# Kernel optimization log

Measured on AMD Instinct MI355X. Metric: run time of the kernel, lower is better.

Reference implementation:

```python
import jax, jax.numpy as jnp
import numpy as np

N_NODES = 50000
N_EDGES = 600000
N_GRAPHS = 512
HID = 128
LAT = 64
L = 4
BN_EPS = 1e-5


def _gelu(x):
    return jax.nn.gelu(x, approximate=False)


def _bn(x, g, b):
    m = jnp.mean(x, axis=0)
    v = jnp.var(x, axis=0)
    return (x - m) * jax.lax.rsqrt(v + BN_EPS) * g + b


def setup_inputs() -> dict:
    key = jax.random.key(0)
    ks = jax.random.split(key, 8)
    x = jax.random.normal(ks[0], (N_NODES, HID), dtype=jnp.float32)
    edge_index = jax.random.randint(ks[1], (2, N_EDGES), 0, N_NODES, dtype=jnp.int64 if jax.config.jax_enable_x64 else jnp.int32)
    batch = jnp.sort(jax.random.randint(ks[2], (N_NODES,), 0, N_GRAPHS))
    scale = 1.0 / np.sqrt(HID)
    return {
        "x": x,
        "edge_index": edge_index,
        "batch": batch,
        "input_bn_g": jnp.ones((HID,), jnp.float32),
        "input_bn_b": jnp.zeros((HID,), jnp.float32),
        "eps": jnp.zeros((L,), jnp.float32),
        "fc1_w": jax.random.normal(ks[3], (L, HID, HID), jnp.float32) * scale,
        "fc1_b": jnp.zeros((L, HID), jnp.float32),
        "bn1_g": jnp.ones((L, HID), jnp.float32),
        "bn1_b": jnp.zeros((L, HID), jnp.float32),
        "fc2_w": jax.random.normal(ks[4], (L, HID, HID), jnp.float32) * scale,
        "fc2_b": jnp.zeros((L, HID), jnp.float32),
        "bn_g": jnp.ones((L, HID), jnp.float32),
        "bn_b": jnp.zeros((L, HID), jnp.float32),
        "att_weight": jax.random.normal(ks[5], (L, HID), jnp.float32),
        "pool_weight": jnp.ones((3,), jnp.float32),
        "fcA_w": jax.random.normal(ks[6], (HID, HID), jnp.float32) * scale,
        "fcA_b": jnp.zeros((HID,), jnp.float32),
        "ln_g": jnp.ones((HID,), jnp.float32),
        "ln_b": jnp.zeros((HID,), jnp.float32),
        "fcB_w": jax.random.normal(ks[7], (HID, LAT), jnp.float32) * scale,
        "fcB_b": jnp.zeros((LAT,), jnp.float32),
    }


def reference(x, edge_index, batch, input_bn_g, input_bn_b, eps, fc1_w, fc1_b,
              bn1_g, bn1_b, fc2_w, fc2_b, bn_g, bn_b, att_weight, pool_weight,
              fcA_w, fcA_b, ln_g, ln_b, fcB_w, fcB_b):
    src, dst = edge_index[0], edge_index[1]
    x = _bn(x, input_bn_g, input_bn_b)  # input BatchNorm (batch stats)
    hidden_states = []
    for l in range(L):
        # GINConv: (1+eps)*x_i + sum_{j->i} x_j, then GatedResidualMLP
        agg = jax.ops.segment_sum(x[src], dst, num_segments=N_NODES)
        h = (1.0 + eps[l]) * x + agg
        h = _gelu(_bn(h @ fc1_w[l] + fc1_b[l], bn1_g[l], bn1_b[l]))
        h = h @ fc2_w[l] + fc2_b[l]
        h = _gelu(_bn(h, bn_g[l], bn_b[l]))
        hidden_states.append(h)
        x = h
    # JumpingKnowledge attention over layers
    x_all = jnp.stack(hidden_states, axis=0)               # [L, N, H]
    scores = jnp.mean(x_all * att_weight[:, None, :], -1)  # [L, N]
    alpha = jax.nn.softmax(scores, axis=0)
    x = jnp.sum(x_all * alpha[..., None], axis=0)          # [N, H]
    # fused add/mean/max pooling by graph id
    pw = jax.nn.softmax(pool_weight)
    sums = jax.ops.segment_sum(x, batch, num_segments=N_GRAPHS)
    cnt = jax.ops.segment_sum(jnp.ones((N_NODES, 1), x.dtype), batch, num_segments=N_GRAPHS)
    mean = sums / jnp.maximum(cnt, 1.0)
    mx = jax.ops.segment_max(x, batch, num_segments=N_GRAPHS)
    mx = jnp.where(cnt > 0, mx, 0.0)
    pooled = sums * pw[0] + mean * pw[1] + mx * pw[2]      # [G, H]
    out = pooled @ fcA_w + fcA_b
    mu = jnp.mean(out, -1, keepdims=True)
    var = jnp.var(out, -1, keepdims=True)
    out = (out - mu) * jax.lax.rsqrt(var + 1e-5) * ln_g + ln_b
    out = _gelu(out) + pooled
    return out @ fcB_w + fcB_b                              # [G, latent]
```

## Files before the change

### kernel.cpp

```cpp
#include <hip/hip_runtime.h>
#include <math.h>

#define N_NODES 50000
#define N_EDGES 600000
#define N_GRAPHS 512
#define HID 128
#define LAT 64
#define NL 4
#define SSTR 16
#define SSET 4096
#define N_TILES 3125
#define TLD 72

typedef __attribute__((ext_vector_type(8))) __bf16 bf16x8;
typedef __attribute__((ext_vector_type(4))) float f32x4;

union Chunk {
    bf16x8 v;
    uint4 u4;
    ushort us[8];
};

__device__ __forceinline__ float gelu_exact(float x) {
    return 0.5f * x * (1.0f + erff(x * 0.70710678118654752f));
}
__device__ __forceinline__ float gelu_fast(float x) {
    float ax = fabsf(x) * 0.70710678118654752f;
    float t = __builtin_amdgcn_rcpf(fmaf(0.3275911f, ax, 1.0f));
    float p = t * (0.254829592f +
              t * (-0.284496736f +
              t * (1.421413741f +
              t * (-1.453152027f + t * 1.061405429f))));
    float e = __expf(-ax * ax);
    float erfv = 1.0f - p * e;
    float erfs = copysignf(erfv, x);
    return 0.5f * x * (1.0f + erfs);
}
__device__ __forceinline__ float bf2f(ushort h) {
    return __uint_as_float(((unsigned int)h) << 16);
}
__device__ __forceinline__ ushort f2bf(float f) {
    unsigned int u = __float_as_uint(f);
    unsigned int r = (u + 0x7FFFu + ((u >> 16) & 1u)) >> 16;
    return (ushort)r;
}

__device__ __forceinline__ void part_range(int p, int& r0, int& r1) {
    r0 = (p * N_NODES) >> 8;
    r1 = ((p + 1) * N_NODES) >> 8;
}
__device__ __forceinline__ void sub_range(int p, int j, int& s0, int& s1) {
    int r0, r1;
    part_range(p, r0, r1);
    int len = r1 - r0;
    s0 = r0 + ((len * j) >> 3);
    s1 = r0 + ((len * (j + 1)) >> 3);
}

__global__ __launch_bounds__(256) void wt_build(const float* __restrict__ fc1w,
                                                const float* __restrict__ fc2w,
                                                ushort* __restrict__ Wt) {
    int i = blockIdx.x * 256 + threadIdx.x;
    if (i >= 8 * HID * HID) return;
    int g = i >> 14;
    int rem = i & 16383;
    int n = rem >> 7, k = rem & 127;
    const float* W = (g < 4) ? (fc1w + (long)g * HID * HID) : (fc2w + (long)(g - 4) * HID * HID);
    Wt[i] = f2bf(W[k * HID + n]);
}

__global__ __launch_bounds__(256) void col_stats(const float* __restrict__ X,
                                                 float* __restrict__ stats) {
    __shared__ float sh[2048];
    int t = threadIdx.x;
    int tx = t & 31, ty = t >> 5;
    float s[4] = {0, 0, 0, 0}, q[4] = {0, 0, 0, 0};
    const int nTiles = (N_NODES + 63) / 64;
    for (int tile = blockIdx.x; tile < nTiles; tile += gridDim.x) {
        int r0 = tile * 64;
#pragma unroll
        for (int i = 0; i < 8; ++i) {
            int r = r0 + ty + 8 * i;
            int rc = min(r, N_NODES - 1);
            float4 v = *(const float4*)(X + (long)rc * HID + 4 * tx);
            float w = (r < N_NODES) ? 1.f : 0.f;
            float x0 = v.x * w, x1 = v.y * w, x2 = v.z * w, x3 = v.w * w;
// ... 26 lines not shown
                                                    ushort* __restrict__ Y,
                                                    const float* __restrict__ stats,
                                                    const float* __restrict__ g,
                                                    const float* __restrict__ b) {
    __shared__ float scL[HID], sfL[HID];
    int t = threadIdx.x;
    if (t < HID) {
        const float invN = 1.0f / (float)N_NODES;
        float mean = stats[t * SSTR] * invN;
        float var = stats[(HID + t) * SSTR] * invN - mean * mean;
        float s = g[t] * rsqrtf(var + 1e-5f);
        scL[t] = s;
        sfL[t] = b[t] - mean * s;
    }
    __syncthreads();
    int c4 = (t & 31) * 4;
    float sc[4], sf[4];
#pragma unroll
    for (int j = 0; j < 4; ++j) { sc[j] = scL[c4 + j]; sf[j] = sfL[c4 + j]; }
    int s0, s1;
    sub_range(blockIdx.x & 255, blockIdx.x >> 8, s0, s1);
    int c0 = s0 * 32, c1 = s1 * 32;
    for (int i = c0 + t; i < c1; i += 256) {
        float4 v = ((const float4*)X)[i];
        ushort4 w;
        w.x = f2bf(v.x * sc[0] + sf[0]);
        w.y = f2bf(v.y * sc[1] + sf[1]);
        w.z = f2bf(v.z * sc[2] + sf[2]);
        w.w = f2bf(v.w * sc[3] + sf[3]);
        ((ushort4*)Y)[i] = w;
    }
}

__global__ __launch_bounds__(256) void bn_apply_bf(const ushort* __restrict__ X,
                                                   ushort* __restrict__ Y,
                                                   const float* __restrict__ stats,
                                                   const float* __restrict__ g,
                                                   const float* __restrict__ b) {
    __shared__ float scL[HID], sfL[HID];
    int t = threadIdx.x;
    if (t < HID) {
        const float invN = 1.0f / (float)N_NODES;
        float mean = stats[t * SSTR] * invN;
        float var = stats[(HID + t) * SSTR] * invN - mean * mean;
        float s = g[t] * rsqrtf(var + 1e-5f);
        scL[t] = s;
        sfL[t] = b[t] - mean * s;
    }
    __syncthreads();
    int c8 = (t & 15) * 8;
    float sc[8], sf[8];
#pragma unroll
    for (int j = 0; j < 8; ++j) { sc[j] = scL[c8 + j]; sf[j] = sfL[c8 + j]; }
    int s0, s1;
    sub_range(blockIdx.x & 255, blockIdx.x >> 8, s0, s1);
    int c0 = s0 * 16, c1 = s1 * 16;
    for (int i = c0 + t; i < c1; i += 256) {
        Chunk ch;
        ch.u4 = ((const uint4*)X)[i];
#pragma unroll
        for (int j = 0; j < 8; ++j) {
            float f = bf2f(ch.us[j]) * sc[j] + sf[j];
            ch.us[j] = f2bf(gelu_fast(f));
        }
        ((uint4*)Y)[i] = ch.u4;
    }
}

__global__ __launch_bounds__(256) void csr_count(const int* __restrict__ dst,
                                                 int* __restrict__ counts) {
    int e = blockIdx.x * blockDim.x + threadIdx.x;
    if (e >= N_EDGES) return;
    atomicAdd(counts + dst[e], 1);
}

__global__ __launch_bounds__(256) void scan_pass1(const int* __restrict__ counts,
                                                  int* __restrict__ offs,
                                                  int* __restrict__ bsum) {
    __shared__ int sh[256];
    int t = threadIdx.x;
    int i = blockIdx.x * 256 + t;
    int v = (i < N_NODES) ? counts[i] : 0;
    sh[t] = v;
    __syncthreads();
    for (int off = 1; off < 256; off <<= 1) {
        int a = (t >= off) ? sh[t - off] : 0;
        __syncthreads();
        sh[t] += a;
        __syncthreads();
    }
    if (i < N_NODES) offs[i] = sh[t] - v;
    if (t == 255) bsum[blockIdx.x] = sh[255];
}

__global__ __launch_bounds__(256) void scan_pass2(int* __restrict__ bsum, int nblk) {
    __shared__ int sh[256];
    int t = threadIdx.x;
    int v = (t < nblk) ? bsum[t] : 0;
    sh[t] = v;
    __syncthreads();
    for (int off = 1; off < 256; off <<= 1) {
        int a = (t >= off) ? sh[t - off] : 0;
        __syncthreads();
        sh[t] += a;
        __syncthreads();
    }
    if (t < nblk) bsum[t] = sh[t] - v;
}

__global__ __launch_bounds__(256) void scan_pass3(int* __restrict__ offs,
                                                  const int* __restrict__ bsum,
                                                  int* __restrict__ cursor) {
    int i = blockIdx.x * 256 + threadIdx.x;
    if (i >= N_NODES) return;
    int o = offs[i] + bsum[blockIdx.x];
    offs[i] = o;
    cursor[i] = o;
}

__global__ __launch_bounds__(256) void csr_fill(const int* __restrict__ src,
                                                const int* __restrict__ dst,
                                                int* __restrict__ cursor,
                                                int* __restrict__ csr) {
    int e = blockIdx.x * blockDim.x + threadIdx.x;
    if (e >= N_EDGES) return;
    int pos = atomicAdd(cursor + dst[e], 1);
    csr[pos] = src[e];
}

__global__ __launch_bounds__(256) void gin_gather_bf(const ushort* __restrict__ Xbf,
                                                     ushort* __restrict__ Hp,
                                                     const int* __restrict__ offs,
                                                     const int* __restrict__ counts,
                                                     const int* __restrict__ csr,
                                                     const float* __restrict__ eps, int l) {
    int t = threadIdx.x;
    int tx = t & 31;
    int g = t >> 5;
    int s0, s1;
    sub_range(blockIdx.x & 255, blockIdx.x >> 8, s0, s1);
    float ev = 1.0f + eps[l];
    for (int node = s0 + g; node < s1; node += 8) {
        ushort4 sv = *(const ushort4*)(Xbf + (long)node * HID + 4 * tx);
        float a0 = bf2f(sv.x) * ev, a1 = bf2f(sv.y) * ev;
        float a2 = bf2f(sv.z) * ev, a3 = bf2f(sv.w) * ev;
        int o = offs[node];
        int d = counts[node];
        int k = 0;
        for (; k + 8 <= d; k += 8) {
            int si[8];
#pragma unroll
            for (int j = 0; j < 8; ++j) si[j] = csr[o + k + j];
            ushort4 v[8];
#pragma unroll
            for (int j = 0; j < 8; ++j)
                v[j] = *(const ushort4*)(Xbf + (long)si[j] * HID + 4 * tx);
#pragma unroll
            for (int j = 0; j < 8; ++j) {
                a0 += bf2f(v[j].x); a1 += bf2f(v[j].y);
                a2 += bf2f(v[j].z); a3 += bf2f(v[j].w);
            }
        }
        for (; k + 4 <= d; k += 4) {
            int si[4];
#pragma unroll
            for (int j = 0; j < 4; ++j) si[j] = csr[o + k + j];
#pragma unroll
            for (int j = 0; j < 4; ++j) {
                ushort4 v = *(const ushort4*)(Xbf + (long)si[j] * HID + 4 * tx);
                a0 += bf2f(v.x); a1 += bf2f(v.y); a2 += bf2f(v.z); a3 += bf2f(v.w);
            }
        }
        for (; k < d; ++k) {
            int s = csr[o + k];
            ushort4 v = *(const ushort4*)(Xbf + (long)s * HID + 4 * tx);
            a0 += bf2f(v.x); a1 += bf2f(v.y); a2 += bf2f(v.z); a3 += bf2f(v.w);
        }
        ushort4 w;
        w.x = f2bf(a0); w.y = f2bf(a1); w.z = f2bf(a2); w.w = f2bf(a3);
        *(ushort4*)(Hp + (long)node * HID + 4 * tx) = w;
    }
}

__global__ __launch_bounds__(256, 1) void gemm_persist(
    const ushort* __restrict__ Abf, const ushort* __restrict__ Wt,
    const float* __restrict__ bias, ushort* __restrict__ Cbf,
    const float* __restrict__ statsIn, const float* __restrict__ gIn,
    const float* __restrict__ bIn, int applyIn, float* __restrict__ statsOut) {
    __shared__ float scL[HID], sfL[HID];
    __shared__ __align__(16) ushort T[4][16 * TLD];
    __shared__ float shs[8 * 64];
    int t = threadIdx.x;
    if (applyIn && t < HID) {
        const float invN = 1.0f / (float)N_NODES;
        float mean = statsIn[t * SSTR] * invN;
        float var = statsIn[(HID + t) * SSTR] * invN - mean * mean;
        float s = gIn[t] * rsqrtf(var + 1e-5f);
        scL[t] = s;
        sfL[t] = bIn[t] - mean * s;
    }
    __syncthreads();

    int w = t >> 6, lane = t & 63;
    int m = lane & 15, q = lane >> 4;
    int c2 = w & 1, r2 = w >> 1;
    ushort* Tw = T[w];

    const ushort* Wh = Wt + (long)(c2 * 64) * HID;
    bf16x8 Bfrag[4][4];
#pragma unroll
    for (int nt = 0; nt < 4; ++nt)
#pragma unroll
        for (int kc = 0; kc < 4; ++kc)
            Bfrag[nt][kc] = *(const bf16x8*)(Wh + (nt * 16 + m) * HID + kc * 32 + q * 8);

    float bias4[4];
#pragma unroll
    for (int nt = 0; nt < 4; ++nt) bias4[nt] = bias[c2 * 64 + nt * 16 + m];

    float s_col[4], q_col[4];
#pragma unroll
    for (int nt = 0; nt < 4; ++nt) { s_col[nt] = 0.f; q_col[nt] = 0.f; }

    int t0 = (blockIdx.x * N_TILES) >> 8;
    int t1 = ((blockIdx.x + 1) * N_TILES) >> 8;

    int tile = t0 + r2;
    Chunk Ac[4];
    if (tile < t1) {
        const ushort* arow = Abf + (long)(tile * 16 + m) * HID + q * 8;
#pragma unroll
        for (int kc = 0; kc < 4; ++kc) Ac[kc].u4 = *(const uint4*)(arow + kc * 32);
    }
    while (tile < t1) {
        int nxt = tile + 2;
        Chunk An[4];
        if (nxt < t1) {
            const ushort* arow = Abf + (long)(nxt * 16 + m) * HID + q * 8;
#pragma unroll
            for (int kc = 0; kc < 4; ++kc) An[kc].u4 = *(const uint4*)(arow + kc * 32);
        }
        if (applyIn) {
#pragma unroll
            for (int kc = 0; kc < 4; ++kc)
#pragma unroll
                for (int j = 0; j < 8; ++j) {
                    int k = kc * 32 + q * 8 + j;
                    float f = bf2f(Ac[kc].us[j]) * scL[k] + sfL[k];
                    Ac[kc].us[j] = f2bf(gelu_fast(f));
                }
        }
        f32x4 acc[4];
#pragma unroll
        for (int nt = 0; nt < 4; ++nt) acc[nt] = (f32x4){0.f, 0.f, 0.f, 0.f};
#pragma unroll
        for (int kc = 0; kc < 4; ++kc)
#pragma unroll
            for (int nt = 0; nt < 4; ++nt)
// ... 17 lines not shown
            int row = slot >> 3, off = slot & 7;
            uint4 vv = *(const uint4*)(Tw + row * TLD + off * 8);
            *(uint4*)(Cbf + cbase + (long)row * HID + off * 8) = vv;
        }
        tile = nxt;
#pragma unroll
        for (int kc = 0; kc < 4; ++kc) Ac[kc] = An[kc];
    }

#pragma unroll
    for (int nt = 0; nt < 4; ++nt) {
        s_col[nt] += __shfl_xor(s_col[nt], 16);
        s_col[nt] += __shfl_xor(s_col[nt], 32);
        q_col[nt] += __shfl_xor(q_col[nt], 16);
        q_col[nt] += __shfl_xor(q_col[nt], 32);
    }
    if (q == 0) {
#pragma unroll
        for (int nt = 0; nt < 4; ++nt) {
            shs[w * 64 + nt * 16 + m] = s_col[nt];
            shs[256 + w * 64 + nt * 16 + m] = q_col[nt];
        }
    }
    __syncthreads();
    if (t < HID) {
        int half = t >> 6, lc = t & 63;
        float a = shs[half * 64 + lc] + shs[(2 + half) * 64 + lc];
        float b = shs[256 + half * 64 + lc] + shs[256 + (2 + half) * 64 + lc];
        atomicAdd(statsOut + t * SSTR, a);
        atomicAdd(statsOut + (HID + t) * SSTR, b);
    }
}

__global__ __launch_bounds__(256) void jk_attn_bf(const ushort* __restrict__ H0,
                                                  const ushort* __restrict__ H1,
                                                  const ushort* __restrict__ H2,
                                                  const ushort* __restrict__ H3,
                                                  const float* __restrict__ att,
                                                  float* __restrict__ Y) {
    int t = threadIdx.x;
    int lane = t & 63, w = t >> 6;
    int s0, s1;
    sub_range(blockIdx.x & 255, blockIdx.x >> 8, s0, s1);
    const ushort* Hs[4] = {H0, H1, H2, H3};
    float2 av[4];
#pragma unroll
    for (int l = 0; l < 4; ++l) av[l] = *(const float2*)(att + l * HID + 2 * lane);
    for (int node = s0 + w; node < s1; node += 4) {
        float hx[4], hy[4], sc[4];
#pragma unroll
        for (int l = 0; l < 4; ++l) {
            unsigned int u = *(const unsigned int*)(Hs[l] + (long)node * HID + 2 * lane);
            float vx = bf2f((ushort)(u & 0xFFFF));
            float vy = bf2f((ushort)(u >> 16));
            hx[l] = vx; hy[l] = vy;
            float p = vx * av[l].x + vy * av[l].y;
#pragma unroll
            for (int off = 32; off > 0; off >>= 1) p += __shfl_xor(p, off);
            sc[l] = p * (1.0f / HID);
        }
        float mm = fmaxf(fmaxf(sc[0], sc[1]), fmaxf(sc[2], sc[3]));
        float e[4], se = 0.f;
#pragma unroll
        for (int l = 0; l < 4; ++l) { e[l] = expf(sc[l] - mm); se += e[l]; }
        float inv = 1.0f / se;
        float ox = 0.f, oy = 0.f;
#pragma unroll
        for (int l = 0; l < 4; ++l) {
            float a = e[l] * inv;
            ox += a * hx[l];
            oy += a * hy[l];
        }
        *(float2*)(Y + (long)node * HID + 2 * lane) = make_float2(ox, oy);
    }
}

__global__ void graph_ranges(const int* __restrict__ batch, int* __restrict__ gstart,
                             int* __restrict__ gend) {
    int n = blockIdx.x * blockDim.x + threadIdx.x;
    if (n >= N_NODES) return;
    int b = batch[n];
    if (n == 0 || batch[n - 1] != b) gstart[b] = n;
    if (n == N_NODES - 1 || batch[n + 1] != b) gend[b] = n + 1;
}

__global__ __launch_bounds__(128) void pool_kernel(const float* __restrict__ X,
                                                   const int* __restrict__ gstart,
                                                   const int* __restrict__ gend,
                                                   const float* __restrict__ pw,
                                                   float* __restrict__ pooled) {
    int g = blockIdx.x;
    int f = threadIdx.x;
    float w0 = pw[0], w1 = pw[1], w2 = pw[2];
    float m = fmaxf(w0, fmaxf(w1, w2));
    float e0 = expf(w0 - m), e1 = expf(w1 - m), e2 = expf(w2 - m);
    float inv = 1.0f / (e0 + e1 + e2);
    e0 *= inv; e1 *= inv; e2 *= inv;
    int s = gstart[g], e = gend[g];
    float sum = 0.f, mx = -INFINITY;
    for (int n = s; n < e; ++n) {
        float v = X[(long)n * HID + f];
        sum += v;
        mx = fmaxf(mx, v);
    }
    int cnt = e - s;
    float mean = cnt > 0 ? sum / (float)cnt : 0.f;
    float mxv = cnt > 0 ? mx : 0.f;
    pooled[g * HID + f] = sum * e0 + mean * e1 + mxv * e2;
}

__global__ __launch_bounds__(128) void head_kernel(const float* __restrict__ pooled,
                                                   const float* __restrict__ fcAw,
                                                   const float* __restrict__ fcAb,
                                                   const float* __restrict__ lng,
                                                   const float* __restrict__ lnb,
                                                   const float* __restrict__ fcBw,
                                                   const float* __restrict__ fcBb,
                                                   float* __restrict__ out) {
    __shared__ float p[HID], q[HID], red[HID];
    int g = blockIdx.x, j = threadIdx.x;
    p[j] = pooled[g * HID + j];
    __syncthreads();
    float acc = fcAb[j];
    for (int k = 0; k < HID; ++k) acc += p[k] * fcAw[k * HID + j];
    red[j] = acc;
    __syncthreads();
    for (int off = 64; off > 0; off >>= 1) {
        if (j < off) red[j] += red[j + off];
        __syncthreads();
    }
    float mean = red[0] * (1.0f / HID);
    __syncthreads();
    float d = acc - mean;
    red[j] = d * d;
    __syncthreads();
    for (int off = 64; off > 0; off >>= 1) {
        if (j < off) red[j] += red[j + off];
        __syncthreads();
    }
    float var = red[0] * (1.0f / HID);
    float y = d * rsqrtf(var + 1e-5f) * lng[j] + lnb[j];
// ... 8 lines not shown

extern "C" void kernel_launch(void* const* d_in, const int* in_sizes, int n_in,
                              void* d_out, int out_size, void* d_ws, size_t ws_size,
                              hipStream_t stream) {
    const float* x = (const float*)d_in[0];
    const int* ei = (const int*)d_in[1];
    const int* src = ei;
    const int* dst = ei + N_EDGES;
    const int* batch = (const int*)d_in[2];
    const float* ibn_g = (const float*)d_in[3];
    const float* ibn_b = (const float*)d_in[4];
    const float* eps = (const float*)d_in[5];
    const float* fc1w = (const float*)d_in[6];
    const float* fc1b = (const float*)d_in[7];
    const float* bn1g = (const float*)d_in[8];
    const float* bn1b = (const float*)d_in[9];
    const float* fc2w = (const float*)d_in[10];
    const float* fc2b = (const float*)d_in[11];
    const float* bng = (const float*)d_in[12];
    const float* bnb = (const float*)d_in[13];
    const float* att = (const float*)d_in[14];
    const float* pw = (const float*)d_in[15];
    const float* fcAw = (const float*)d_in[16];
    const float* fcAb = (const float*)d_in[17];
    const float* lng = (const float*)d_in[18];
    const float* lnb = (const float*)d_in[19];
    const float* fcBw = (const float*)d_in[20];
    const float* fcBb = (const float*)d_in[21];
    float* out = (float*)d_out;

    const size_t NH = (size_t)N_NODES * HID;
    char* w8 = (char*)d_ws;
    ushort* x0bf = (ushort*)w8;     w8 += NH * 2;
    ushort* hprebf = (ushort*)w8;   w8 += NH * 2;
    ushort* z1bf = (ushort*)w8;     w8 += NH * 2;
    ushort* Hlbf[NL];
    for (int l = 0; l < NL; ++l) { Hlbf[l] = (ushort*)w8; w8 += NH * 2; }
    float* ztmp = (float*)w8;       w8 += NH * 4;
    float* statsAll = (float*)w8;   w8 += (size_t)9 * SSET * 4;
    float* pooled = (float*)w8;     w8 += (size_t)N_GRAPHS * HID * 4;
    int* gstart = (int*)w8;         w8 += N_GRAPHS * 4;
    int* gend = (int*)w8;           w8 += N_GRAPHS * 4;
    int* counts = (int*)w8;         w8 += N_NODES * 4;
    int* offs = (int*)w8;           w8 += N_NODES * 4;
    int* cursor = (int*)w8;         w8 += N_NODES * 4;
    int* bsum = (int*)w8;           w8 += 256 * 4;
    int* csr = (int*)w8;            w8 += (size_t)N_EDGES * 4;
    ushort* WtBf = (ushort*)w8;     w8 += (size_t)8 * HID * HID * 2;

    const int nodeBlocks = (N_NODES + 255) / 256;
    const int edgeBlocks = (N_EDGES + 255) / 256;

    wt_build<<<512, 256, 0, stream>>>(fc1w, fc2w, WtBf);

    hipMemsetAsync(counts, 0, N_NODES * sizeof(int), stream);
    csr_count<<<edgeBlocks, 256, 0, stream>>>(dst, counts);
    scan_pass1<<<nodeBlocks, 256, 0, stream>>>(counts, offs, bsum);
    scan_pass2<<<1, 256, 0, stream>>>(bsum, nodeBlocks);
    scan_pass3<<<nodeBlocks, 256, 0, stream>>>(offs, bsum, cursor);
    csr_fill<<<edgeBlocks, 256, 0, stream>>>(src, dst, cursor, csr);

    hipMemsetAsync(statsAll, 0, (size_t)9 * SSET * sizeof(float), stream);

    col_stats<<<256, 256, 0, stream>>>(x, statsAll);
    bn_apply_f32<<<2048, 256, 0, stream>>>(x, x0bf, statsAll, ibn_g, ibn_b);

    const ushort* xin = x0bf;
    for (int l = 0; l < NL; ++l) {
        float* st1 = statsAll + (size_t)(1 + 2 * l) * SSET;
        float* st2 = statsAll + (size_t)(2 + 2 * l) * SSET;
        gin_gather_bf<<<2048, 256, 0, stream>>>(xin, hprebf, offs, counts, csr, eps, l);
        gemm_persist<<<256, 256, 0, stream>>>(hprebf, WtBf + (size_t)l * HID * HID,
                                              fc1b + l * HID, z1bf,
                                              nullptr, nullptr, nullptr, 0, st1);
        gemm_persist<<<256, 256, 0, stream>>>(z1bf, WtBf + (size_t)(4 + l) * HID * HID,
                                              fc2b + l * HID, hprebf,
                                              st1, bn1g + l * HID, bn1b + l * HID, 1, st2);
        bn_apply_bf<<<2048, 256, 0, stream>>>(hprebf, Hlbf[l], st2, bng + l * HID,
                                              bnb + l * HID);
        xin = Hlbf[l];
    }

    jk_attn_bf<<<2048, 256, 0, stream>>>(Hlbf[0], Hlbf[1], Hlbf[2], Hlbf[3], att, ztmp);

    hipMemsetAsync(gstart, 0, 2 * N_GRAPHS * sizeof(int), stream);
    graph_ranges<<<nodeBlocks, 256, 0, stream>>>(batch, gstart, gend);
    pool_kernel<<<N_GRAPHS, 128, 0, stream>>>(ztmp, gstart, gend, pw, pooled);

    head_kernel<<<N_GRAPHS, 128, 0, stream>>>(pooled, fcAw, fcAb, lng, lnb, fcBw, fcBb, out);
}
```

Before: 557.8 us.

## Fuse GIN neighbor gather into first per-layer GEMM with MFMA

Replaces the separate gather kernel plus first persistent GEMM with one kernel in which each thread aggregates a full node row (its own features scaled by 1+eps, plus its neighbors) straight into MFMA A-fragments, then multiplies by register-resident weight fragments and accumulates BN statistics. This removes the write and re-read of the aggregated hidden buffer and one launch per layer. In exchange, each block redoes its weight-fragment loads, uses launch_bounds(256,1), and gathers with one thread per row at 16-byte width, which may hide latency worse than the old warp-per-node gather and is hit by degree imbalance within a wave.

```diff
diff --git a/kernel.cpp b/kernel.cpp
--- a/kernel.cpp
+++ b/kernel.cpp
@@ -10,6 +10,7 @@
 #define SSTR 16
 #define SSET 4096
 #define N_TILES 3125
+#define N_GG 1563
 #define TLD 72
 
 typedef __attribute__((ext_vector_type(8))) __bf16 bf16x8;
@@ -45,13 +46,9 @@
     return (ushort)r;
 }
 
-__device__ __forceinline__ void part_range(int p, int& r0, int& r1) {
-    r0 = (p * N_NODES) >> 8;
-    r1 = ((p + 1) * N_NODES) >> 8;
-}
 __device__ __forceinline__ void sub_range(int p, int j, int& s0, int& s1) {
-    int r0, r1;
-    part_range(p, r0, r1);
+    int r0 = (p * N_NODES) >> 8;
+    int r1 = ((p + 1) * N_NODES) >> 8;
     int len = r1 - r0;
     s0 = r0 + ((len * j) >> 3);
     s1 = r0 + ((len * (j + 1)) >> 3);
@@ -240,57 +237,141 @@
     csr[pos] = src[e];
 }
 
-__global__ __launch_bounds__(256) void gin_gather_bf(const ushort* __restrict__ Xbf,
-                                                     ushort* __restrict__ Hp,
-                                                     const int* __restrict__ offs,
-                                                     const int* __restrict__ counts,
-                                                     const int* __restrict__ csr,
-                                                     const float* __restrict__ eps, int l) {
+__global__ __launch_bounds__(256, 1) void gather_gemm(
+    const ushort* __restrict__ Xbf, const int* __restrict__ offs,
+    const int* __restrict__ counts, const int* __restrict__ csr,
+    const float* __restrict__ eps, int l,
+    const ushort* __restrict__ Wt, const float* __restrict__ bias,
+    ushort* __restrict__ Cbf, float* __restrict__ statsOut) {
+    __shared__ __align__(16) ushort T[4][16 * TLD];
+    __shared__ float shs[8 * 64];
     int t = threadIdx.x;
-    int tx = t & 31;
-    int g = t >> 5;
-    int s0, s1;
-    sub_range(blockIdx.x & 255, blockIdx.x >> 8, s0, s1);
+    int w = t >> 6, lane = t & 63;
+    int m = lane & 15, q = lane >> 4;
+    int c2 = w & 1, r2 = w >> 1;
+    ushort* Tw = T[w];
+
+    const ushort* Wh = Wt + (long)(c2 * 64) * HID;
+    bf16x8 Bfrag[4][4];
+#pragma unroll
+    for (int nt = 0; nt < 4; ++nt)
+#pragma unroll
+        for (int kc = 0; kc < 4; ++kc)
+            Bfrag[nt][kc] = *(const bf16x8*)(Wh + (nt * 16 + m) * HID + kc * 32 + q * 8);
+
+    float bias4[4];
+#pragma unroll
+    for (int nt = 0; nt < 4; ++nt) bias4[nt] = bias[c2 * 64 + nt * 16 + m];
+
     float ev = 1.0f + eps[l];
-    for (int node = s0 + g; node < s1; node += 8) {
-        ushort4 sv = *(const ushort4*)(Xbf + (long)node * HID + 4 * tx);
-        float a0 = bf2f(sv.x) * ev, a1 = bf2f(sv.y) * ev;
-        float a2 = bf2f(sv.z) * ev, a3 = bf2f(sv.w) * ev;
-        int o = offs[node];
-        int d = counts[node];
-        int k = 0;
-        for (; k + 8 <= d; k += 8) {
-            int si[8];
-#pragma unroll
-            for (int j = 0; j < 8; ++j) si[j] = csr[o + k + j];
-            ushort4 v[8];
+    int rbase = blockIdx.x * 32 + r2 * 16;
+    int row = rbase + m;
+    int valid = row < N_NODES;
+    int rowc = valid ? row : N_NODES - 1;
+
+    float accf[4][8];
+    {
+        const ushort* xr = Xbf + (long)rowc * HID + q * 8;
+        Chunk ch[4];
+#pragma unroll
+        for (int kc = 0; kc < 4; ++kc) ch[kc].u4 = *(const uint4*)(xr + kc * 32);
+#pragma unroll
+        for (int kc = 0; kc < 4; ++kc)
+#pragma unroll
+            for (int j = 0; j < 8; ++j) accf[kc][j] = bf2f(ch[kc].us[j]) * ev;
+    }
+    int d = valid ? counts[row] : 0;
+    int o = valid ? offs[row] : 0;
+    int k = 0;
+    for (; k + 2 <= d; k += 2) {
+        int s0 = csr[o + k], s1 = csr[o + k + 1];
+        const ushort* p0 = Xbf + (long)s0 * HID + q * 8;
+        const ushort* p1 = Xbf + (long)s1 * HID + q * 8;
+        Chunk a0[4], a1[4];
+#pragma unroll
+        for (int kc = 0; kc < 4; ++kc) {
+            a0[kc].u4 = *(const uint4*)(p0 + kc * 32);
+            a1[kc].u4 = *(const uint4*)(p1 + kc * 32);
+        }
+#pragma unroll
+        for (int kc = 0; kc < 4; ++kc)
 #pragma unroll
             for (int j = 0; j < 8; ++j)
-                v[j] = *(const ushort4*)(Xbf + (long)si[j] * HID + 4 * tx);
-#pragma unroll
-            for (int j = 0; j < 8; ++j) {
-                a0 += bf2f(v[j].x); a1 += bf2f(v[j].y);
-                a2 += bf2f(v[j].z); a3 += bf2f(v[j].w);
+                accf[kc][j] += bf2f(a0[kc].us[j]) + bf2f(a1[kc].us[j]);
+    }
+    if (k < d) {
+        int s0 = csr[o + k];
+        const ushort* p0 = Xbf + (long)s0 * HID + q * 8;
+        Chunk a0[4];
+#pragma unroll
+        for (int kc = 0; kc < 4; ++kc) a0[kc].u4 = *(const uint4*)(p0 + kc * 32);
+#pragma unroll
+        for (int kc = 0; kc < 4; ++kc)
+#pragma unroll
+            for (int j = 0; j < 8; ++j) accf[kc][j] += bf2f(a0[kc].us[j]);
+    }
+
+    Chunk Af[4];
+#pragma unroll
+    for (int kc = 0; kc < 4; ++kc)
+#pragma unroll
+        for (int j = 0; j < 8; ++j) Af[kc].us[j] = f2bf(accf[kc][j]);
+
+    f32x4 acc[4];
+#pragma unroll
+    for (int nt = 0; nt < 4; ++nt) acc[nt] = (f32x4){0.f, 0.f, 0.f, 0.f};
+#pragma unroll
+    for (int kc = 0; kc < 4; ++kc)
+#pragma unroll
+        for (int nt = 0; nt < 4; ++nt)
+            acc[nt] = __builtin_amdgcn_mfma_f32_16x16x32_bf16(Af[kc].v, Bfrag[nt][kc],
+                                                              acc[nt], 0, 0, 0);
+
+    float s_col[4] = {0, 0, 0, 0}, q_col[4] = {0, 0, 0, 0};
+#pragma unroll
+    for (int nt = 0; nt < 4; ++nt) {
+        int col = nt * 16 + m;
+#pragma unroll
+        for (int r = 0; r < 4; ++r) {
+            float z = acc[nt][r] + bias4[nt];
+            Tw[(q * 4 + r) * TLD + col] = f2bf(z);
+            if (rbase + q * 4 + r < N_NODES) {
+                s_col[nt] += z;
+                q_col[nt] += z * z;
             }
         }
-        for (; k + 4 <= d; k += 4) {
-            int si[4];
-#pragma unroll
-            for (int j = 0; j < 4; ++j) si[j] = csr[o + k + j];
-#pragma unroll
-            for (int j = 0; j < 4; ++j) {
-                ushort4 v = *(const ushort4*)(Xbf + (long)si[j] * HID + 4 * tx);
-                a0 += bf2f(v.x); a1 += bf2f(v.y); a2 += bf2f(v.z); a3 += bf2f(v.w);
-            }
-        }
-        for (; k < d; ++k) {
-            int s = csr[o + k];
-            ushort4 v = *(const ushort4*)(Xbf + (long)s * HID + 4 * tx);
-            a0 += bf2f(v.x); a1 += bf2f(v.y); a2 += bf2f(v.z); a3 += bf2f(v.w);
-        }
-        ushort4 w;
-        w.x = f2bf(a0); w.y = f2bf(a1); w.z = f2bf(a2); w.w = f2bf(a3);
-        *(ushort4*)(Hp + (long)node * HID + 4 * tx) = w;
+    }
+#pragma unroll
+    for (int i = 0; i < 2; ++i) {
+        int slot = i * 64 + lane;
+        int rrow = slot >> 3, off = slot & 7;
+        if (rbase + rrow < N_NODES) {
+            uint4 vv = *(const uint4*)(Tw + rrow * TLD + off * 8);
+            *(uint4*)(Cbf + (long)(rbase + rrow) * HID + c2 * 64 + off * 8) = vv;
+        }
+    }
+
+#pragma unroll
+    for (int nt = 0; nt < 4; ++nt) {
+        s_col[nt] += __shfl_xor(s_col[nt], 16);
+        s_col[nt] += __shfl_xor(s_col[nt], 32);
+        q_col[nt] += __shfl_xor(q_col[nt], 16);
+        q_col[nt] += __shfl_xor(q_col[nt], 32);
+    }
+    if (q == 0) {
+#pragma unroll
+        for (int nt = 0; nt < 4; ++nt) {
+            shs[w * 64 + nt * 16 + m] = s_col[nt];
+            shs[256 + w * 64 + nt * 16 + m] = q_col[nt];
+        }
+    }
+    __syncthreads();
+    if (t < HID) {
+        int half = t >> 6, lc = t & 63;
+        float a = shs[half * 64 + lc] + shs[(2 + half) * 64 + lc];
+        float b = shs[256 + half * 64 + lc] + shs[256 + (2 + half) * 64 + lc];
+        atomicAdd(statsOut + t * SSTR, a);
+        atomicAdd(statsOut + (HID + t) * SSTR, b);
     }
 }
 
@@ -568,7 +649,7 @@
     const size_t NH = (size_t)N_NODES * HID;
     char* w8 = (char*)d_ws;
     ushort* x0bf = (ushort*)w8;     w8 += NH * 2;
-    ushort* hprebf = (ushort*)w8;   w8 += NH * 2;
+    ushort* z2bf = (ushort*)w8;     w8 += NH * 2;
     ushort* z1bf = (ushort*)w8;     w8 += NH * 2;
     ushort* Hlbf[NL];
     for (int l = 0; l < NL; ++l) { Hlbf[l] = (ushort*)w8; w8 += NH * 2; }
@@ -605,14 +686,13 @@
     for (int l = 0; l < NL; ++l) {
         float* st1 = statsAll + (size_t)(1 + 2 * l) * SSET;
         float* st2 = statsAll + (size_t)(2 + 2 * l) * SSET;
-        gin_gather_bf<<<2048, 256, 0, stream>>>(xin, hprebf, offs, counts, csr, eps, l);
-        gemm_persist<<<256, 256, 0, stream>>>(hprebf, WtBf + (size_t)l * HID * HID,
-                                              fc1b + l * HID, z1bf,
-                                              nullptr, nullptr, nullptr, 0, st1);
+        gather_gemm<<<N_GG, 256, 0, stream>>>(xin, offs, counts, csr, eps, l,
+                                              WtBf + (size_t)l * HID * HID,
+                                              fc1b + l * HID, z1bf, st1);
         gemm_persist<<<256, 256, 0, stream>>>(z1bf, WtBf + (size_t)(4 + l) * HID * HID,
-                                              fc2b + l * HID, hprebf,
+                                              fc2b + l * HID, z2bf,
                                               st1, bn1g + l * HID, bn1b + l * HID, 1, st2);
-        bn_apply_bf<<<2048, 256, 0, stream>>>(hprebf, Hlbf[l], st2, bng + l * HID,
+        bn_apply_bf<<<2048, 256, 0, stream>>>(z2bf, Hlbf[l], st2, bng + l * HID,
                                               bnb + l * HID);
         xin = Hlbf[l];
     }
```

Result: slower. 755.2 us (+35.4%).

## Fuse post-layer BatchNorm+GELU into neighbor gather and JK attention consumers

Applied to the files above, without the earlier changes.

Removes the standalone bn_apply_bf pass after each layer. The second GEMM now writes its pre-normalization output, and the next layer's gather applies BN+GELU to every gathered neighbor row on the fly. JK attention applies the same normalization to all four layers. This saves one read+write pass over the node features per layer, but recomputes GELU for each edge (about 12x per node) instead of once per node, and shrinks the gather unroll from 8 to 4 in the BN path.

```diff
diff --git a/kernel.cpp b/kernel.cpp
--- a/kernel.cpp
+++ b/kernel.cpp
@@ -45,13 +45,9 @@
     return (ushort)r;
 }
 
-__device__ __forceinline__ void part_range(int p, int& r0, int& r1) {
-    r0 = (p * N_NODES) >> 8;
-    r1 = ((p + 1) * N_NODES) >> 8;
-}
 __device__ __forceinline__ void sub_range(int p, int j, int& s0, int& s1) {
-    int r0, r1;
-    part_range(p, r0, r1);
+    int r0 = (p * N_NODES) >> 8;
+    int r1 = ((p + 1) * N_NODES) >> 8;
     int len = r1 - r0;
     s0 = r0 + ((len * j) >> 3);
     s1 = r0 + ((len * (j + 1)) >> 3);
@@ -144,41 +140,6 @@
     }
 }
 
-__global__ __launch_bounds__(256) void bn_apply_bf(const ushort* __restrict__ X,
-                                                   ushort* __restrict__ Y,
-                                                   const float* __restrict__ stats,
-                                                   const float* __restrict__ g,
-                                                   const float* __restrict__ b) {
-    __shared__ float scL[HID], sfL[HID];
-    int t = threadIdx.x;
-    if (t < HID) {
-        const float invN = 1.0f / (float)N_NODES;
-        float mean = stats[t * SSTR] * invN;
-        float var = stats[(HID + t) * SSTR] * invN - mean * mean;
-        float s = g[t] * rsqrtf(var + 1e-5f);
-        scL[t] = s;
-        sfL[t] = b[t] - mean * s;
-    }
-    __syncthreads();
-    int c8 = (t & 15) * 8;
-    float sc[8], sf[8];
-#pragma unroll
-    for (int j = 0; j < 8; ++j) { sc[j] = scL[c8 + j]; sf[j] = sfL[c8 + j]; }
-    int s0, s1;
-    sub_range(blockIdx.x & 255, blockIdx.x >> 8, s0, s1);
-    int c0 = s0 * 16, c1 = s1 * 16;
-    for (int i = c0 + t; i < c1; i += 256) {
-        Chunk ch;
-        ch.u4 = ((const uint4*)X)[i];
-#pragma unroll
-        for (int j = 0; j < 8; ++j) {
-            float f = bf2f(ch.us[j]) * sc[j] + sf[j];
-            ch.us[j] = f2bf(gelu_fast(f));
-        }
-        ((uint4*)Y)[i] = ch.u4;
-    }
-}
-
 __global__ __launch_bounds__(256) void csr_count(const int* __restrict__ dst,
                                                  int* __restrict__ counts) {
     int e = blockIdx.x * blockDim.x + threadIdx.x;
@@ -240,57 +201,106 @@
     csr[pos] = src[e];
 }
 
-__global__ __launch_bounds__(256) void gin_gather_bf(const ushort* __restrict__ Xbf,
+__global__ __launch_bounds__(256) void gin_gather_bn(const ushort* __restrict__ Zbf,
                                                      ushort* __restrict__ Hp,
                                                      const int* __restrict__ offs,
                                                      const int* __restrict__ counts,
                                                      const int* __restrict__ csr,
-                                                     const float* __restrict__ eps, int l) {
+                                                     const float* __restrict__ eps, int l,
+                                                     const float* __restrict__ stats,
+                                                     const float* __restrict__ g,
+                                                     const float* __restrict__ b,
+                                                     int applyBn) {
     int t = threadIdx.x;
     int tx = t & 31;
-    int g = t >> 5;
+    int grp = t >> 5;
     int s0, s1;
     sub_range(blockIdx.x & 255, blockIdx.x >> 8, s0, s1);
     float ev = 1.0f + eps[l];
-    for (int node = s0 + g; node < s1; node += 8) {
-        ushort4 sv = *(const ushort4*)(Xbf + (long)node * HID + 4 * tx);
-        float a0 = bf2f(sv.x) * ev, a1 = bf2f(sv.y) * ev;
-        float a2 = bf2f(sv.z) * ev, a3 = bf2f(sv.w) * ev;
-        int o = offs[node];
-        int d = counts[node];
-        int k = 0;
-        for (; k + 8 <= d; k += 8) {
-            int si[8];
-#pragma unroll
-            for (int j = 0; j < 8; ++j) si[j] = csr[o + k + j];
-            ushort4 v[8];
-#pragma unroll
-            for (int j = 0; j < 8; ++j)
-                v[j] = *(const ushort4*)(Xbf + (long)si[j] * HID + 4 * tx);
-#pragma unroll
-            for (int j = 0; j < 8; ++j) {
-                a0 += bf2f(v[j].x); a1 += bf2f(v[j].y);
-                a2 += bf2f(v[j].z); a3 += bf2f(v[j].w);
+
+    float sc[4], sf[4];
+    if (applyBn) {
+        const float invN = 1.0f / (float)N_NODES;
+#pragma unroll
+        for (int j = 0; j < 4; ++j) {
+            int c = 4 * tx + j;
+            float mean = stats[c * SSTR] * invN;
+            float var = stats[(HID + c) * SSTR] * invN - mean * mean;
+            float s = g[c] * rsqrtf(var + 1e-5f);
+            sc[j] = s;
+            sf[j] = b[c] - mean * s;
+        }
+    }
+
+    if (applyBn) {
+        for (int node = s0 + grp; node < s1; node += 8) {
+            ushort4 sv = *(const ushort4*)(Zbf + (long)node * HID + 4 * tx);
+            float a0 = gelu_fast(bf2f(sv.x) * sc[0] + sf[0]) * ev;
+            float a1 = gelu_fast(bf2f(sv.y) * sc[1] + sf[1]) * ev;
+            float a2 = gelu_fast(bf2f(sv.z) * sc[2] + sf[2]) * ev;
+            float a3 = gelu_fast(bf2f(sv.w) * sc[3] + sf[3]) * ev;
+            int o = offs[node];
+            int d = counts[node];
+            int k = 0;
+            for (; k + 4 <= d; k += 4) {
+                int si[4];
+#pragma unroll
+                for (int j = 0; j < 4; ++j) si[j] = csr[o + k + j];
+                ushort4 v[4];
+#pragma unroll
+                for (int j = 0; j < 4; ++j)
+                    v[j] = *(const ushort4*)(Zbf + (long)si[j] * HID + 4 * tx);
+#pragma unroll
+                for (int j = 0; j < 4; ++j) {
+                    a0 += gelu_fast(bf2f(v[j].x) * sc[0] + sf[0]);
+                    a1 += gelu_fast(bf2f(v[j].y) * sc[1] + sf[1]);
+                    a2 += gelu_fast(bf2f(v[j].z) * sc[2] + sf[2]);
+                    a3 += gelu_fast(bf2f(v[j].w) * sc[3] + sf[3]);
+                }
             }
-        }
-        for (; k + 4 <= d; k += 4) {
-            int si[4];
-#pragma unroll
-            for (int j = 0; j < 4; ++j) si[j] = csr[o + k + j];
-#pragma unroll
-            for (int j = 0; j < 4; ++j) {
-                ushort4 v = *(const ushort4*)(Xbf + (long)si[j] * HID + 4 * tx);
+            for (; k < d; ++k) {
+                int s = csr[o + k];
+                ushort4 v = *(const ushort4*)(Zbf + (long)s * HID + 4 * tx);
+                a0 += gelu_fast(bf2f(v.x) * sc[0] + sf[0]);
+                a1 += gelu_fast(bf2f(v.y) * sc[1] + sf[1]);
+                a2 += gelu_fast(bf2f(v.z) * sc[2] + sf[2]);
+                a3 += gelu_fast(bf2f(v.w) * sc[3] + sf[3]);
+            }
+            ushort4 w;
+            w.x = f2bf(a0); w.y = f2bf(a1); w.z = f2bf(a2); w.w = f2bf(a3);
+            *(ushort4*)(Hp + (long)node * HID + 4 * tx) = w;
+        }
+    } else {
+        for (int node = s0 + grp; node < s1; node += 8) {
+            ushort4 sv = *(const ushort4*)(Zbf + (long)node * HID + 4 * tx);
+            float a0 = bf2f(sv.x) * ev, a1 = bf2f(sv.y) * ev;
+            float a2 = bf2f(sv.z) * ev, a3 = bf2f(sv.w) * ev;
+            int o = offs[node];
+            int d = counts[node];
+            int k = 0;
+            for (; k + 8 <= d; k += 8) {
+                int si[8];
+#pragma unroll
+                for (int j = 0; j < 8; ++j) si[j] = csr[o + k + j];
+                ushort4 v[8];
+#pragma unroll
+                for (int j = 0; j < 8; ++j)
+                    v[j] = *(const ushort4*)(Zbf + (long)si[j] * HID + 4 * tx);
+#pragma unroll
+                for (int j = 0; j < 8; ++j) {
+                    a0 += bf2f(v[j].x); a1 += bf2f(v[j].y);
+                    a2 += bf2f(v[j].z); a3 += bf2f(v[j].w);
+                }
+            }
+            for (; k < d; ++k) {
+                int s = csr[o + k];
+                ushort4 v = *(const ushort4*)(Zbf + (long)s * HID + 4 * tx);
                 a0 += bf2f(v.x); a1 += bf2f(v.y); a2 += bf2f(v.z); a3 += bf2f(v.w);
             }
-        }
-        for (; k < d; ++k) {
-            int s = csr[o + k];
-            ushort4 v = *(const ushort4*)(Xbf + (long)s * HID + 4 * tx);
-            a0 += bf2f(v.x); a1 += bf2f(v.y); a2 += bf2f(v.z); a3 += bf2f(v.w);
-        }
-        ushort4 w;
-        w.x = f2bf(a0); w.y = f2bf(a1); w.z = f2bf(a2); w.w = f2bf(a3);
-        *(ushort4*)(Hp + (long)node * HID + 4 * tx) = w;
+            ushort4 w;
+            w.x = f2bf(a0); w.y = f2bf(a1); w.z = f2bf(a2); w.w = f2bf(a3);
+            *(ushort4*)(Hp + (long)node * HID + 4 * tx) = w;
+        }
     }
 }
 
@@ -419,37 +429,56 @@
     }
 }
 
-__global__ __launch_bounds__(256) void jk_attn_bf(const ushort* __restrict__ H0,
-                                                  const ushort* __restrict__ H1,
-                                                  const ushort* __restrict__ H2,
-                                                  const ushort* __restrict__ H3,
+__global__ __launch_bounds__(256) void jk_attn_bn(const ushort* __restrict__ Z0,
+                                                  const ushort* __restrict__ Z1,
+                                                  const ushort* __restrict__ Z2,
+                                                  const ushort* __restrict__ Z3,
+                                                  const float* __restrict__ statsAll,
+                                                  const float* __restrict__ bng,
+                                                  const float* __restrict__ bnb,
                                                   const float* __restrict__ att,
                                                   float* __restrict__ Y) {
     int t = threadIdx.x;
     int lane = t & 63, w = t >> 6;
     int s0, s1;
     sub_range(blockIdx.x & 255, blockIdx.x >> 8, s0, s1);
-    const ushort* Hs[4] = {H0, H1, H2, H3};
+    const ushort* Zs[4] = {Z0, Z1, Z2, Z3};
+    const float invN = 1.0f / (float)N_NODES;
     float2 av[4];
-#pragma unroll
-    for (int l = 0; l < 4; ++l) av[l] = *(const float2*)(att + l * HID + 2 * lane);
+    float sc[4][2], sf[4][2];
+#pragma unroll
+    for (int l = 0; l < 4; ++l) {
+        av[l] = *(const float2*)(att + l * HID + 2 * lane);
+        const float* st = statsAll + (size_t)(2 + 2 * l) * SSET;
+        const float* g = bng + l * HID;
+        const float* b = bnb + l * HID;
+#pragma unroll
+        for (int j = 0; j < 2; ++j) {
+            int c = 2 * lane + j;
+            float mean = st[c * SSTR] * invN;
+            float var = st[(HID + c) * SSTR] * invN - mean * mean;
+            float s = g[c] * rsqrtf(var + 1e-5f);
+            sc[l][j] = s;
+            sf[l][j] = b[c] - mean * s;
+        }
+    }
     for (int node = s0 + w; node < s1; node += 4) {
-        float hx[4], hy[4], sc[4];
+        float hx[4], hy[4], scr[4];
 #pragma unroll
         for (int l = 0; l < 4; ++l) {
-            unsigned int u = *(const unsigned int*)(Hs[l] + (long)node * HID + 2 * lane);
-            float vx = bf2f((ushort)(u & 0xFFFF));
-            float vy = bf2f((ushort)(u >> 16));
+            unsigned int u = *(const unsigned int*)(Zs[l] + (long)node * HID + 2 * lane);
+            float vx = gelu_fast(bf2f((ushort)(u & 0xFFFF)) * sc[l][0] + sf[l][0]);
+            float vy = gelu_fast(bf2f((ushort)(u >> 16)) * sc[l][1] + sf[l][1]);
             hx[l] = vx; hy[l] = vy;
             float p = vx * av[l].x + vy * av[l].y;
 #pragma unroll
             for (int off = 32; off > 0; off >>= 1) p += __shfl_xor(p, off);
-            sc[l] = p * (1.0f / HID);
-        }
-        float mm = fmaxf(fmaxf(sc[0], sc[1]), fmaxf(sc[2], sc[3]));
+            scr[l] = p * (1.0f / HID);
+        }
+        float mm = fmaxf(fmaxf(scr[0], scr[1]), fmaxf(scr[2], scr[3]));
         float e[4], se = 0.f;
 #pragma unroll
-        for (int l = 0; l < 4; ++l) { e[l] = expf(sc[l] - mm); se += e[l]; }
+        for (int l = 0; l < 4; ++l) { e[l] = expf(scr[l] - mm); se += e[l]; }
         float inv = 1.0f / se;
         float ox = 0.f, oy = 0.f;
 #pragma unroll
@@ -570,8 +599,8 @@
     ushort* x0bf = (ushort*)w8;     w8 += NH * 2;
     ushort* hprebf = (ushort*)w8;   w8 += NH * 2;
     ushort* z1bf = (ushort*)w8;     w8 += NH * 2;
-    ushort* Hlbf[NL];
-    for (int l = 0; l < NL; ++l) { Hlbf[l] = (ushort*)w8; w8 += NH * 2; }
+    ushort* Zl[NL];
+    for (int l = 0; l < NL; ++l) { Zl[l] = (ushort*)w8; w8 += NH * 2; }
     float* ztmp = (float*)w8;       w8 += NH * 4;
     float* statsAll = (float*)w8;   w8 += (size_t)9 * SSET * 4;
     float* pooled = (float*)w8;     w8 += (size_t)N_GRAPHS * HID * 4;
@@ -605,19 +634,24 @@
     for (int l = 0; l < NL; ++l) {
         float* st1 = statsAll + (size_t)(1 + 2 * l) * SSET;
         float* st2 = statsAll + (size_t)(2 + 2 * l) * SSET;
-        gin_gather_bf<<<2048, 256, 0, stream>>>(xin, hprebf, offs, counts, csr, eps, l);
+        const float* stPrev = statsAll + (size_t)(2 * l) * SSET;
+        gin_gather_bn<<<2048, 256, 0, stream>>>(
+            xin, hprebf, offs, counts, csr, eps, l,
+            (l > 0) ? stPrev : nullptr,
+            (l > 0) ? (bng + (l - 1) * HID) : nullptr,
+            (l > 0) ? (bnb + (l - 1) * HID) : nullptr,
+            l > 0 ? 1 : 0);
         gemm_persist<<<256, 256, 0, stream>>>(hprebf, WtBf + (size_t)l * HID * HID,
                                               fc1b + l * HID, z1bf,
                                               nullptr, nullptr, nullptr, 0, st1);
         gemm_persist<<<256, 256, 0, stream>>>(z1bf, WtBf + (size_t)(4 + l) * HID * HID,
-                                              fc2b + l * HID, hprebf,
+                                              fc2b + l * HID, Zl[l],
                                               st1, bn1g + l * HID, bn1b + l * HID, 1, st2);
-        bn_apply_bf<<<2048, 256, 0, stream>>>(hprebf, Hlbf[l], st2, bng + l * HID,
-                                              bnb + l * HID);
-        xin = Hlbf[l];
-    }
-
-    jk_attn_bf<<<2048, 256, 0, stream>>>(Hlbf[0], Hlbf[1], Hlbf[2], Hlbf[3], att, ztmp);
+        xin = Zl[l];
+    }
+
+    jk_attn_bn<<<2048, 256, 0, stream>>>(Zl[0], Zl[1], Zl[2], Zl[3], statsAll, bng, bnb,
+                                         att, ztmp);
 
     hipMemsetAsync(gstart, 0, 2 * N_GRAPHS * sizeof(int), stream);
     graph_ranges<<<nodeBlocks, 256, 0, stream>>>(batch, gstart, gend);
```

New measurement: 682.7 us. 22.4% more time.

## Fuse JK attention with graph pooling via atomics and double GEMM grid

Applied to the files above, without the earlier changes.

Merges the jumping-knowledge attention kernel with the segment sum/max pooling. Each wave accumulates running sums and maxima per graph over its contiguous node range and flushes them with atomic add and an atomic float max. This removes the fp32 intermediate node tensor write and read. The persistent GEMM grid is also doubled to 512 blocks, and the fc2 output now goes to a separate buffer instead of reusing the gather buffer. The risks are atomic contention and nondeterministic summation order.

```diff
diff --git a/kernel.cpp b/kernel.cpp
--- a/kernel.cpp
+++ b/kernel.cpp
@@ -44,14 +44,14 @@
     unsigned int r = (u + 0x7FFFu + ((u >> 16) & 1u)) >> 16;
     return (ushort)r;
 }
-
-__device__ __forceinline__ void part_range(int p, int& r0, int& r1) {
-    r0 = (p * N_NODES) >> 8;
-    r1 = ((p + 1) * N_NODES) >> 8;
-}
+__device__ __forceinline__ void atomicMaxF(float* addr, float v) {
+    if (v >= 0.f) atomicMax((int*)addr, __float_as_int(v));
+    else atomicMin((unsigned int*)addr, __float_as_uint(v));
+}
+
 __device__ __forceinline__ void sub_range(int p, int j, int& s0, int& s1) {
-    int r0, r1;
-    part_range(p, r0, r1);
+    int r0 = (p * N_NODES) >> 8;
+    int r1 = ((p + 1) * N_NODES) >> 8;
     int len = r1 - r0;
     s0 = r0 + ((len * j) >> 3);
     s1 = r0 + ((len * (j + 1)) >> 3);
@@ -248,11 +248,11 @@
                                                      const float* __restrict__ eps, int l) {
     int t = threadIdx.x;
     int tx = t & 31;
-    int g = t >> 5;
+    int grp = t >> 5;
     int s0, s1;
     sub_range(blockIdx.x & 255, blockIdx.x >> 8, s0, s1);
     float ev = 1.0f + eps[l];
-    for (int node = s0 + g; node < s1; node += 8) {
+    for (int node = s0 + grp; node < s1; node += 8) {
         ushort4 sv = *(const ushort4*)(Xbf + (long)node * HID + 4 * tx);
         float a0 = bf2f(sv.x) * ev, a1 = bf2f(sv.y) * ev;
         float a2 = bf2f(sv.z) * ev, a3 = bf2f(sv.w) * ev;
@@ -334,8 +334,8 @@
 #pragma unroll
     for (int nt = 0; nt < 4; ++nt) { s_col[nt] = 0.f; q_col[nt] = 0.f; }
 
-    int t0 = (blockIdx.x * N_TILES) >> 8;
-    int t1 = ((blockIdx.x + 1) * N_TILES) >> 8;
+    int t0 = (blockIdx.x * N_TILES) >> 9;
+    int t1 = ((blockIdx.x + 1) * N_TILES) >> 9;
 
     int tile = t0 + r2;
     Chunk Ac[4];
@@ -419,22 +419,51 @@
     }
 }
 
-__global__ __launch_bounds__(256) void jk_attn_bf(const ushort* __restrict__ H0,
-                                                  const ushort* __restrict__ H1,
-                                                  const ushort* __restrict__ H2,
-                                                  const ushort* __restrict__ H3,
-                                                  const float* __restrict__ att,
-                                                  float* __restrict__ Y) {
+__global__ __launch_bounds__(256) void pool_init(float* __restrict__ psum,
+                                                 float* __restrict__ pmax) {
+    int i = blockIdx.x * 256 + threadIdx.x;
+    if (i >= N_GRAPHS * HID) return;
+    psum[i] = 0.f;
+    pmax[i] = -INFINITY;
+}
+
+__global__ __launch_bounds__(256) void jk_pool(const ushort* __restrict__ H0,
+                                               const ushort* __restrict__ H1,
+                                               const ushort* __restrict__ H2,
+                                               const ushort* __restrict__ H3,
+                                               const float* __restrict__ att,
+                                               const int* __restrict__ batch,
+                                               float* __restrict__ psum,
+                                               float* __restrict__ pmax) {
     int t = threadIdx.x;
     int lane = t & 63, w = t >> 6;
-    int s0, s1;
-    sub_range(blockIdx.x & 255, blockIdx.x >> 8, s0, s1);
+    int r0 = (blockIdx.x * N_NODES) >> 9;
+    int r1 = ((blockIdx.x + 1) * N_NODES) >> 9;
+    int len = r1 - r0;
+    int a0 = r0 + ((len * w) >> 2);
+    int a1 = r0 + ((len * (w + 1)) >> 2);
     const ushort* Hs[4] = {H0, H1, H2, H3};
     float2 av[4];
 #pragma unroll
     for (int l = 0; l < 4; ++l) av[l] = *(const float2*)(att + l * HID + 2 * lane);
-    for (int node = s0 + w; node < s1; node += 4) {
-        float hx[4], hy[4], sc[4];
+
+    int curg = -1;
+    float sx = 0.f, sy = 0.f, mx = -INFINITY, my = -INFINITY;
+    for (int node = a0; node < a1; ++node) {
+        int g = batch[node];
+        if (g != curg) {
+            if (curg >= 0) {
+                float* ps = psum + (long)curg * HID + 2 * lane;
+                float* pm = pmax + (long)curg * HID + 2 * lane;
+                atomicAdd(ps, sx);
+                atomicAdd(ps + 1, sy);
+                atomicMaxF(pm, mx);
+                atomicMaxF(pm + 1, my);
+            }
+            curg = g;
+            sx = 0.f; sy = 0.f; mx = -INFINITY; my = -INFINITY;
+        }
+        float hx[4], hy[4], scr[4];
 #pragma unroll
         for (int l = 0; l < 4; ++l) {
             unsigned int u = *(const unsigned int*)(Hs[l] + (long)node * HID + 2 * lane);
@@ -444,12 +473,12 @@
             float p = vx * av[l].x + vy * av[l].y;
 #pragma unroll
             for (int off = 32; off > 0; off >>= 1) p += __shfl_xor(p, off);
-            sc[l] = p * (1.0f / HID);
-        }
-        float mm = fmaxf(fmaxf(sc[0], sc[1]), fmaxf(sc[2], sc[3]));
+            scr[l] = p * (1.0f / HID);
+        }
+        float mm = fmaxf(fmaxf(scr[0], scr[1]), fmaxf(scr[2], scr[3]));
         float e[4], se = 0.f;
 #pragma unroll
-        for (int l = 0; l < 4; ++l) { e[l] = expf(sc[l] - mm); se += e[l]; }
+        for (int l = 0; l < 4; ++l) { e[l] = expf(scr[l] - mm); se += e[l]; }
         float inv = 1.0f / se;
         float ox = 0.f, oy = 0.f;
 #pragma unroll
@@ -458,8 +487,37 @@
             ox += a * hx[l];
             oy += a * hy[l];
         }
-        *(float2*)(Y + (long)node * HID + 2 * lane) = make_float2(ox, oy);
-    }
+        sx += ox; sy += oy;
+        mx = fmaxf(mx, ox); my = fmaxf(my, oy);
+    }
+    if (curg >= 0) {
+        float* ps = psum + (long)curg * HID + 2 * lane;
+        float* pm = pmax + (long)curg * HID + 2 * lane;
+        atomicAdd(ps, sx);
+        atomicAdd(ps + 1, sy);
+        atomicMaxF(pm, mx);
+        atomicMaxF(pm + 1, my);
+    }
+}
+
+__global__ __launch_bounds__(128) void pool_finalize(const float* __restrict__ psum,
+                                                     const float* __restrict__ pmax,
+                                                     const int* __restrict__ gstart,
+                                                     const int* __restrict__ gend,
+                                                     const float* __restrict__ pw,
+                                                     float* __restrict__ pooled) {
+    int g = blockIdx.x, f = threadIdx.x;
+    float w0 = pw[0], w1 = pw[1], w2 = pw[2];
+    float m = fmaxf(w0, fmaxf(w1, w2));
+    float e0 = expf(w0 - m), e1 = expf(w1 - m), e2 = expf(w2 - m);
+    float inv = 1.0f / (e0 + e1 + e2);
+    e0 *= inv; e1 *= inv; e2 *= inv;
+    int cnt = gend[g] - gstart[g];
+    float s = psum[g * HID + f];
+    float mx = pmax[g * HID + f];
+    float mean = cnt > 0 ? s / (float)cnt : 0.f;
+    float mxv = cnt > 0 ? mx : 0.f;
+    pooled[g * HID + f] = s * e0 + mean * e1 + mxv * e2;
 }
 
 __global__ void graph_ranges(const int* __restrict__ batch, int* __restrict__ gstart,
@@ -469,31 +527,6 @@
     int b = batch[n];
     if (n == 0 || batch[n - 1] != b) gstart[b] = n;
     if (n == N_NODES - 1 || batch[n + 1] != b) gend[b] = n + 1;
-}
-
-__global__ __launch_bounds__(128) void pool_kernel(const float* __restrict__ X,
-                                                   const int* __restrict__ gstart,
-                                                   const int* __restrict__ gend,
-                                                   const float* __restrict__ pw,
-                                                   float* __restrict__ pooled) {
-    int g = blockIdx.x;
-    int f = threadIdx.x;
-    float w0 = pw[0], w1 = pw[1], w2 = pw[2];
-    float m = fmaxf(w0, fmaxf(w1, w2));
-    float e0 = expf(w0 - m), e1 = expf(w1 - m), e2 = expf(w2 - m);
-    float inv = 1.0f / (e0 + e1 + e2);
-    e0 *= inv; e1 *= inv; e2 *= inv;
-    int s = gstart[g], e = gend[g];
-    float sum = 0.f, mx = -INFINITY;
-    for (int n = s; n < e; ++n) {
-        float v = X[(long)n * HID + f];
-        sum += v;
-        mx = fmaxf(mx, v);
-    }
-    int cnt = e - s;
-    float mean = cnt > 0 ? sum / (float)cnt : 0.f;
-    float mxv = cnt > 0 ? mx : 0.f;
-    pooled[g * HID + f] = sum * e0 + mean * e1 + mxv * e2;
 }
 
 __global__ __launch_bounds__(128) void head_kernel(const float* __restrict__ pooled,
@@ -570,10 +603,12 @@
     ushort* x0bf = (ushort*)w8;     w8 += NH * 2;
     ushort* hprebf = (ushort*)w8;   w8 += NH * 2;
     ushort* z1bf = (ushort*)w8;     w8 += NH * 2;
+    ushort* z2bf = (ushort*)w8;     w8 += NH * 2;
     ushort* Hlbf[NL];
     for (int l = 0; l < NL; ++l) { Hlbf[l] = (ushort*)w8; w8 += NH * 2; }
-    float* ztmp = (float*)w8;       w8 += NH * 4;
     float* statsAll = (float*)w8;   w8 += (size_t)9 * SSET * 4;
+    float* psum = (float*)w8;       w8 += (size_t)N_GRAPHS * HID * 4;
+    float* pmax = (float*)w8;       w8 += (size_t)N_GRAPHS * HID * 4;
     float* pooled = (float*)w8;     w8 += (size_t)N_GRAPHS * HID * 4;
     int* gstart = (int*)w8;         w8 += N_GRAPHS * 4;
     int* gend = (int*)w8;           w8 += N_GRAPHS * 4;
@@ -606,22 +641,23 @@
         float* st1 = statsAll + (size_t)(1 + 2 * l) * SSET;
         float* st2 = statsAll + (size_t)(2 + 2 * l) * SSET;
         gin_gather_bf<<<2048, 256, 0, stream>>>(xin, hprebf, offs, counts, csr, eps, l);
-        gemm_persist<<<256, 256, 0, stream>>>(hprebf, WtBf + (size_t)l * HID * HID,
+        gemm_persist<<<512, 256, 0, stream>>>(hprebf, WtBf + (size_t)l * HID * HID,
                                               fc1b + l * HID, z1bf,
                                               nullptr, nullptr, nullptr, 0, st1);
-        gemm_persist<<<256, 256, 0, stream>>>(z1bf, WtBf + (size_t)(4 + l) * HID * HID,
-                                              fc2b + l * HID, hprebf,
+        gemm_persist<<<512, 256, 0, stream>>>(z1bf, WtBf + (size_t)(4 + l) * HID * HID,
+                                              fc2b + l * HID, z2bf,
                                               st1, bn1g + l * HID, bn1b + l * HID, 1, st2);
-        bn_apply_bf<<<2048, 256, 0, stream>>>(hprebf, Hlbf[l], st2, bng + l * HID,
+        bn_apply_bf<<<2048, 256, 0, stream>>>(z2bf, Hlbf[l], st2, bng + l * HID,
                                               bnb + l * HID);
         xin = Hlbf[l];
     }
 
-    jk_attn_bf<<<2048, 256, 0, stream>>>(Hlbf[0], Hlbf[1], Hlbf[2], Hlbf[3], att, ztmp);
-
+    pool_init<<<(N_GRAPHS * HID + 255) / 256, 256, 0, stream>>>(psum, pmax);
     hipMemsetAsync(gstart, 0, 2 * N_GRAPHS * sizeof(int), stream);
     graph_ranges<<<nodeBlocks, 256, 0, stream>>>(batch, gstart, gend);
-    pool_kernel<<<N_GRAPHS, 128, 0, stream>>>(ztmp, gstart, gend, pw, pooled);
+    jk_pool<<<512, 256, 0, stream>>>(Hlbf[0], Hlbf[1], Hlbf[2], Hlbf[3], att, batch,
+                                     psum, pmax);
+    pool_finalize<<<N_GRAPHS, 128, 0, stream>>>(psum, pmax, gstart, gend, pw, pooled);
 
     head_kernel<<<N_GRAPHS, 128, 0, stream>>>(pooled, fcAw, fcAb, lng, lnb, fcBw, fcBb, out);
 }
```

Result: slower. 582.7 us (+4.5%).
